# Kernel optimization log

Measured on AMD Instinct MI355X. Metric: run time of the kernel, lower is better.

Reference implementation:

```python
import jax, jax.numpy as jnp
import numpy as np

B, C, H, W, NMAX = 16, 1, 128, 8192, 64


def setup_inputs() -> dict:
    key = jax.random.key(0)
    x = jax.random.normal(key, (B, C, H, W), dtype=jnp.float32)
    # Build realistic non-overlapping, sorted chirp boundaries with numpy.
    rng = np.random.default_rng(0)
    slot = W // NMAX  # 128 columns per chirp slot
    gaps = rng.integers(0, 40, size=(B, NMAX))
    widths = rng.integers(20, slot - 40, size=(B, NMAX))
    starts = np.arange(NMAX)[None, :] * slot + gaps
    ends = starts + widths
    n = rng.integers(48, NMAX + 1, size=(B,)).astype(np.int32)
    xi = np.stack([starts, ends], axis=-1).astype(np.int32)
    valid = np.arange(NMAX)[None, :] < n[:, None]
    xi = xi * valid[:, :, None]  # zero out invalid rows
    return {
        "x": x,
        "xi": jnp.asarray(xi),
        "N": jnp.asarray(n),
        "sep_param": jnp.zeros((1, 1, 1), dtype=jnp.float32),  # learned sep token scalar
    }


def reference(x, xi, N, sep_param):
    """Vectorized TinyBird.compactify_data: remove silence between chirp
    blocks, packing blocks contiguously with 1-column separators.
    Returns (x_new, xi_new). x_new keeps full width W (original truncates
    to data-dependent w_max; padding beyond w_max is zeros, same values)."""
    Bb, Cc, Hh, Ww = x.shape
    nmax = xi.shape[1]
    idx = jnp.arange(nmax, dtype=jnp.int32)[None, :]            # (1, Nmax)
    Nc = N.reshape(Bb, 1).astype(jnp.int32)                      # (B, 1)
    w = jnp.clip(xi[:, :, 1] - xi[:, :, 0], 0, None).astype(jnp.int32)
    valid = idx < Nc                                             # (B, Nmax)
    wv = jnp.where(valid, w, 0)
    csum = jnp.cumsum(wv, axis=1)
    start_new = csum - wv + idx                                  # compressed starts
    end_new = csum + idx                                         # compressed ends
    xi_new = jnp.where(valid[:, :, None],
                       jnp.stack([start_new, end_new], axis=-1), 0).astype(xi.dtype)

    # For every output column j, find which compressed segment it falls in.
    j = jnp.arange(Ww, dtype=jnp.int32)
    big = jnp.int32(Ww + nmax + 2)
    start_search = jnp.where(valid, start_new, big)              # keep sorted
    seg = jax.vmap(lambda s: jnp.searchsorted(s, j, side='right'))(start_search) - 1
    seg = jnp.clip(seg, 0, nmax - 1)                             # (B, W)
    bidx = jnp.arange(Bb)[:, None]
    s_new = start_new[bidx, seg]
    e_new = end_new[bidx, seg]
    seg_valid = valid[bidx, seg]
    in_seg = seg_valid & (j[None, :] >= s_new) & (j[None, :] < e_new)
    is_sep = seg_valid & (j[None, :] == e_new) & (seg < (Nc - 1))
    src = jnp.clip(xi[bidx, seg, 0].astype(jnp.int32) + (j[None, :] - s_new), 0, Ww - 1)
    src_full = jnp.broadcast_to(src[:, None, None, :], (Bb, Cc, Hh, Ww))
    gathered = jnp.take_along_axis(x, src_full, axis=3)          # ragged gather
    sep_val = sep_param[0, 0, 0]                                 # sep_token column value
    x_new = jnp.where(in_seg[:, None, None, :], gathered,
                      jnp.where(is_sep[:, None, None, :], sep_val, jnp.float32(0)))
    return x_new, xi_new
```

## Files before the change

kernel.cpp:

```cpp
#include <hip/hip_runtime.h>

#define Bn 16
#define Hn 128
#define Wn 8192
#define NMAX 64

__global__ __launch_bounds__(256) void row_pack_lds_kernel(
    const float* __restrict__ x, const int* __restrict__ xi,
    const int* __restrict__ N, const float* __restrict__ sep_param,
    float* __restrict__ out, float* __restrict__ out_xi) {
    __shared__ float s_row[Wn];
    __shared__ int s_start[NMAX];
    __shared__ int s_w[NMAX];
    __shared__ int s_src0[NMAX];
    __shared__ int s_n, s_tail, s_wide;

    const int row = blockIdx.x;
    const int b   = row >> 7;
    const int tid = threadIdx.x;

    if (tid < NMAX) {
        int nb = N[b];
        int s0 = xi[(b * NMAX + tid) * 2 + 0];
        int s1 = xi[(b * NMAX + tid) * 2 + 1];
        int w = s1 - s0; if (w < 0) w = 0;
        bool valid = tid < nb;
        int wv = valid ? w : 0;
        int c = wv;
        #pragma unroll
        for (int d = 1; d < 64; d <<= 1) {
            int t = __shfl_up(c, d, 64);
            if (tid >= d) c += t;
        }
        int start_new = c - wv + tid;
        int end_new   = c + tid;
        s_start[tid] = start_new;
        s_w[tid]     = wv;
        s_src0[tid]  = s0;
        unsigned long long wide = __ballot(wv > 127);
        if (tid == 0) {
            s_n = nb;
            s_wide = (wide != 0ULL) ? 1 : 0;
        }
        int last = (nb > 0) ? (nb - 1) : 0;
        if (tid == last) s_tail = (nb > 0) ? end_new : 0;
        if ((row & 127) == 0) {
            out_xi[(b * NMAX + tid) * 2 + 0] = valid ? (float)start_new : 0.0f;
            out_xi[(b * NMAX + tid) * 2 + 1] = valid ? (float)end_new : 0.0f;
        }
    }
    __syncthreads();

    const int nb   = s_n;
    const int tail = s_tail;
    const float sep = sep_param[0];
    const float* __restrict__ xrow = x + (size_t)row * Wn;
    float* __restrict__ orow = out + (size_t)row * Wn;
    const int wave = tid >> 6;
    const int lane = tid & 63;

    float v0[16], v1[16];
    int sg_s[16], sg_wt[16];
    #pragma unroll
    for (int k = 0; k < 16; ++k) {
        const int seg = wave + 4 * k;
        const bool act = seg < nb;
        const int s    = act ? s_start[seg] : 0;
        const int w    = act ? s_w[seg] : 0;
        const int src0 = act ? s_src0[seg] : 0;
        sg_s[k]  = s;
        sg_wt[k] = act ? (w + ((seg < nb - 1) ? 1 : 0)) : 0;
        v0[k] = (lane < w)      ? xrow[src0 + lane]      : sep;
        v1[k] = (lane + 64 < w) ? xrow[src0 + lane + 64] : sep;
    }

    #pragma unroll
    for (int k = 0; k < 16; ++k) {
        if (lane < sg_wt[k])      s_row[sg_s[k] + lane]      = v0[k];
        if (lane + 64 < sg_wt[k]) s_row[sg_s[k] + lane + 64] = v1[k];
    }

    if (s_wide) {
        for (int seg = wave; seg < nb; seg += 4) {
            const int w = s_w[seg];
            const int wtot = w + ((seg < nb - 1) ? 1 : 0);
            for (int l = 128 + lane; l < wtot; l += 64) {
                s_row[s_start[seg] + l] = (l < w) ? xrow[s_src0[seg] + l] : sep;
            }
        }
    }

    const int t4 = (tail + 3) & ~3;
    if (tid < (t4 - tail)) s_row[tail + tid] = 0.0f;
    float4* s_row4 = reinterpret_cast<float4*>(s_row);
    const float4 z4 = make_float4(0.0f, 0.0f, 0.0f, 0.0f);
    for (int i4 = (t4 >> 2) + tid; i4 < (Wn >> 2); i4 += 256) {
        s_row4[i4] = z4;
    }
    __syncthreads();

    float4* orow4 = reinterpret_cast<float4*>(orow);
    #pragma unroll
    for (int g = 0; g < 8; ++g) {
        orow4[g * 256 + tid] = s_row4[g * 256 + tid];
    }
}

extern "C" void kernel_launch(void* const* d_in, const int* in_sizes, int n_in,
                              void* d_out, int out_size, void* d_ws, size_t ws_size,
                              hipStream_t stream) {
    const float* x   = (const float*)d_in[0];
    const int* xi    = (const int*)d_in[1];
    const int* N     = (const int*)d_in[2];
    const float* sep = (const float*)d_in[3];

    float* out_x  = (float*)d_out;
    float* out_xi = (float*)d_out + (size_t)Bn * Hn * Wn;

    row_pack_lds_kernel<<<Bn * Hn, 256, 0, stream>>>(x, xi, N, sep, out_x, out_xi);
}
```

Measured before the change: 114.8 us.

## Split each row into two half-width windows processed by separate blocks

Each block now produces only half of an output row, staging 4096 columns in LDS instead of 8192, and the grid doubles. The smaller LDS footprint lets more blocks reside per CU and gives more blocks overall, which helps hide memory latency. In exchange, every block reruns the per-batch prefix scan and issues predicated loads for segments outside its window. Some source loads near the window boundary are fetched by both halves.

```diff
diff --git a/kernel.cpp b/kernel.cpp
--- a/kernel.cpp
+++ b/kernel.cpp
@@ -4,20 +4,24 @@
 #define Hn 128
 #define Wn 8192
 #define NMAX 64
+#define HALF 4096
 
-__global__ __launch_bounds__(256) void row_pack_lds_kernel(
+__global__ __launch_bounds__(256) void row_pack_win_kernel(
     const float* __restrict__ x, const int* __restrict__ xi,
     const int* __restrict__ N, const float* __restrict__ sep_param,
     float* __restrict__ out, float* __restrict__ out_xi) {
-    __shared__ float s_row[Wn];
+    __shared__ float s_half[HALF];
     __shared__ int s_start[NMAX];
     __shared__ int s_w[NMAX];
     __shared__ int s_src0[NMAX];
     __shared__ int s_n, s_tail, s_wide;
 
-    const int row = blockIdx.x;
-    const int b   = row >> 7;
-    const int tid = threadIdx.x;
+    const int win  = blockIdx.x;
+    const int row  = win >> 1;
+    const int half = win & 1;
+    const int b    = row >> 7;
+    const int W0   = half * HALF;
+    const int tid  = threadIdx.x;
 
     if (tid < NMAX) {
         int nb = N[b];
@@ -44,7 +48,7 @@
         }
         int last = (nb > 0) ? (nb - 1) : 0;
         if (tid == last) s_tail = (nb > 0) ? end_new : 0;
-        if ((row & 127) == 0) {
+        if ((row & 127) == 0 && half == 0) {
             out_xi[(b * NMAX + tid) * 2 + 0] = valid ? (float)start_new : 0.0f;
             out_xi[(b * NMAX + tid) * 2 + 1] = valid ? (float)end_new : 0.0f;
         }
@@ -55,12 +59,12 @@
     const int tail = s_tail;
     const float sep = sep_param[0];
     const float* __restrict__ xrow = x + (size_t)row * Wn;
-    float* __restrict__ orow = out + (size_t)row * Wn;
+    float* __restrict__ orow = out + (size_t)row * Wn + W0;
     const int wave = tid >> 6;
     const int lane = tid & 63;
 
     float v0[16], v1[16];
-    int sg_s[16], sg_wt[16];
+    int sg_base[16], sg_lo[16], sg_hi[16];
     #pragma unroll
     for (int k = 0; k < 16; ++k) {
         const int seg = wave + 4 * k;
@@ -68,41 +72,53 @@
         const int s    = act ? s_start[seg] : 0;
         const int w    = act ? s_w[seg] : 0;
         const int src0 = act ? s_src0[seg] : 0;
-        sg_s[k]  = s;
-        sg_wt[k] = act ? (w + ((seg < nb - 1) ? 1 : 0)) : 0;
-        v0[k] = (lane < w)      ? xrow[src0 + lane]      : sep;
-        v1[k] = (lane + 64 < w) ? xrow[src0 + lane + 64] : sep;
+        const int wt   = act ? (w + ((seg < nb - 1) ? 1 : 0)) : 0;
+        const int base = s - W0;
+        int lo = -base; if (lo < 0) lo = 0;
+        int hi = HALF - base; if (hi > wt) hi = wt;
+        sg_base[k] = base;
+        sg_lo[k]   = lo;
+        sg_hi[k]   = hi;
+        const bool d0 = (lane >= lo) && (lane < hi) && (lane < w);
+        const bool d1 = (lane + 64 >= lo) && (lane + 64 < hi) && (lane + 64 < w);
+        v0[k] = d0 ? xrow[src0 + lane]      : sep;
+        v1[k] = d1 ? xrow[src0 + lane + 64] : sep;
     }
 
     #pragma unroll
     for (int k = 0; k < 16; ++k) {
-        if (lane < sg_wt[k])      s_row[sg_s[k] + lane]      = v0[k];
-        if (lane + 64 < sg_wt[k]) s_row[sg_s[k] + lane + 64] = v1[k];
+        const int l0 = lane, l1 = lane + 64;
+        if (l0 >= sg_lo[k] && l0 < sg_hi[k]) s_half[sg_base[k] + l0] = v0[k];
+        if (l1 >= sg_lo[k] && l1 < sg_hi[k]) s_half[sg_base[k] + l1] = v1[k];
     }
 
     if (s_wide) {
         for (int seg = wave; seg < nb; seg += 4) {
             const int w = s_w[seg];
-            const int wtot = w + ((seg < nb - 1) ? 1 : 0);
-            for (int l = 128 + lane; l < wtot; l += 64) {
-                s_row[s_start[seg] + l] = (l < w) ? xrow[s_src0[seg] + l] : sep;
+            const int wt = w + ((seg < nb - 1) ? 1 : 0);
+            const int base = s_start[seg] - W0;
+            for (int l = 128 + lane; l < wt; l += 64) {
+                const int p = base + l;
+                if (p >= 0 && p < HALF) s_half[p] = (l < w) ? xrow[s_src0[seg] + l] : sep;
             }
         }
     }
 
-    const int t4 = (tail + 3) & ~3;
-    if (tid < (t4 - tail)) s_row[tail + tid] = 0.0f;
-    float4* s_row4 = reinterpret_cast<float4*>(s_row);
+    int twin = tail - W0;
+    if (twin < 0) twin = 0; if (twin > HALF) twin = HALF;
+    const int t4 = (twin + 3) & ~3;
+    if (tid < (t4 - twin)) s_half[twin + tid] = 0.0f;
+    float4* s_half4 = reinterpret_cast<float4*>(s_half);
     const float4 z4 = make_float4(0.0f, 0.0f, 0.0f, 0.0f);
-    for (int i4 = (t4 >> 2) + tid; i4 < (Wn >> 2); i4 += 256) {
-        s_row4[i4] = z4;
+    for (int i4 = (t4 >> 2) + tid; i4 < (HALF >> 2); i4 += 256) {
+        s_half4[i4] = z4;
     }
     __syncthreads();
 
     float4* orow4 = reinterpret_cast<float4*>(orow);
     #pragma unroll
-    for (int g = 0; g < 8; ++g) {
-        orow4[g * 256 + tid] = s_row4[g * 256 + tid];
+    for (int g = 0; g < 4; ++g) {
+        orow4[g * 256 + tid] = s_half4[g * 256 + tid];
     }
 }
 
@@ -117,5 +133,5 @@
     float* out_x  = (float*)d_out;
     float* out_xi = (float*)d_out + (size_t)Bn * Hn * Wn;
 
-    row_pack_lds_kernel<<<Bn * Hn, 256, 0, stream>>>(x, xi, N, sep, out_x, out_xi);
+    row_pack_win_kernel<<<Bn * Hn * 2, 256, 0, stream>>>(x, xi, N, sep, out_x, out_xi);
 }
```

Result: slower. 118.4 us (+3.1%).
